# Optimization experiments

Hardware: AMD Instinct MI355X
Metric: run time of the kernel (lower is better)

## Reference

```python
import jax, jax.numpy as jnp
import numpy as np

EPS = 1e-12  # F.normalize eps

def _unfold3(x):
    # x: [B,C,H,W] -> [B, C*9, H*W], matching F.unfold(kernel=3, padding=1)
    B, C, H, W = x.shape
    xp = jnp.pad(x, ((0, 0), (0, 0), (1, 1), (1, 1)))
    pats = jnp.stack([xp[:, :, i:i + H, j:j + W]
                      for i in range(3) for j in range(3)], axis=2)  # [B,C,9,H,W]
    return pats.reshape(B, C * 9, H * W)

def _fold3(t, H, W):
    # inverse of _unfold3 with overlap-add, matching F.fold(kernel=3, padding=1)
    B, CK, L = t.shape
    C = CK // 9
    t = t.reshape(B, C, 3, 3, H, W)
    out = jnp.zeros((B, C, H + 2, W + 2), t.dtype)
    for i in range(3):
        for j in range(3):
            out = out.at[:, :, i:i + H, j:j + W].add(t[:, :, i, j])
    return out[:, :, 1:1 + H, 1:1 + W]

def setup_inputs() -> dict:
    key = jax.random.key(0)
    kV, kK, kQ = jax.random.split(key, 3)
    B, C, H, W = 4, 64, 64, 64
    return {
        'V': jax.random.normal(kV, (B, C, H, W), dtype=jnp.float32),
        'K': jax.random.normal(kK, (B, C, H, W), dtype=jnp.float32),
        'Q': jax.random.normal(kQ, (B, C, H, W), dtype=jnp.float32),
    }

def reference(V, K, Q):
    B, C, H, W = Q.shape
    Qu = _unfold3(Q)  # [B, C9, L]
    Ku = _unfold3(K)  # [B, C9, L]
    # F.normalize along the feature (C*9) axis for both K (after permute dim=2) and Q (dim=1)
    Kn = Ku / jnp.maximum(jnp.linalg.norm(Ku, axis=1, keepdims=True), EPS)
    Qn = Qu / jnp.maximum(jnp.linalg.norm(Qu, axis=1, keepdims=True), EPS)
    # R[b,k,q] = <Kn[b,:,k], Qn[b,:,q]>  -> [B, L, L]
    R = jnp.einsum('bfk,bfq->bkq', Kn, Qn)
    S = jnp.max(R, axis=1)        # [B, L]
    arg = jnp.argmax(R, axis=1)   # [B, L] best key patch per query position
    Vu = _unfold3(V)              # [B, C9, L]
    idx = jnp.broadcast_to(arg[:, None, :], Vu.shape)
    T_unfold = jnp.take_along_axis(Vu, idx, axis=2)  # gather along patch dim
    T = _fold3(T_unfold, H, W) / 9.0                 # [B, C, H, W]
    S = S.reshape(B, 1, H, W)
    return (S, T)
```

## Files before the change

kernel.cpp:

```cpp
#include <hip/hip_runtime.h>
#include <math.h>

#define HW 4096

typedef short bf16x8 __attribute__((ext_vector_type(8)));
typedef float floatx4 __attribute__((ext_vector_type(4)));
typedef unsigned short u16x8 __attribute__((ext_vector_type(8)));

__device__ __forceinline__ unsigned short f2bf_rne(float x) {
    unsigned int u = __float_as_uint(x);
    unsigned int r = (u + 0x7FFFu + ((u >> 16) & 1u)) >> 16;
    return (unsigned short)r;
}
__device__ __forceinline__ float bf2f(unsigned short h) {
    return __uint_as_float(((unsigned int)h) << 16);
}

__device__ __forceinline__ void gload_lds16(const void* gptr, void* lptr) {
    auto g = (const __attribute__((address_space(1))) unsigned int*)(unsigned long long)(gptr);
    auto l = (__attribute__((address_space(3))) unsigned int*)(unsigned int)(unsigned long long)(lptr);
    __builtin_amdgcn_global_load_lds(g, l, 16, 0, 0);
}

__global__ __launch_bounds__(256)
void prep_kernel(const float* __restrict__ Q, const float* __restrict__ K,
                 const float* __restrict__ V,
                 unsigned short* __restrict__ Aq, unsigned short* __restrict__ Bq,
                 float* __restrict__ VT,
                 float* __restrict__ pix2q, float* __restrict__ pix2k) {
    __shared__ float sT[64][65];
    const int tid = threadIdx.x;
    const int p0 = blockIdx.x * 64;
    const int b = blockIdx.y;
    const int which = blockIdx.z;
    const float* __restrict__ src = (which == 0) ? Q : ((which == 1) ? K : V);

#pragma unroll
    for (int it = 0; it < 16; ++it) {
        int idx = it * 256 + tid;
        int c = idx >> 6, x = idx & 63;
        sT[c][x] = src[((size_t)b * 64 + c) * HW + p0 + x];
    }
    __syncthreads();
    const int pp = tid >> 2, qt = tid & 3;

    if (which == 2) {
        float* dst = VT + ((size_t)b * 4096 + p0 + pp) * 64 + qt * 16;
#pragma unroll
        for (int j = 0; j < 4; ++j) {
            float4 v = make_float4(sT[qt * 16 + 4 * j + 0][pp], sT[qt * 16 + 4 * j + 1][pp],
                                   sT[qt * 16 + 4 * j + 2][pp], sT[qt * 16 + 4 * j + 3][pp]);
            *(float4*)(dst + 4 * j) = v;
        }
        return;
    }

    const int isK = which;
    unsigned short* __restrict__ dst = isK ? Bq : Aq;
    float* __restrict__ pix2 = isK ? pix2k : pix2q;
    const size_t base = ((size_t)b * 4096 + p0 + pp) * 192;
    {
        float sq = 0.f;
        u16x8 hv[2], lv[2];
#pragma unroll
        for (int g = 0; g < 2; ++g)
#pragma unroll
            for (int j = 0; j < 8; ++j) {
                int c = qt * 16 + g * 8 + j;
                float x = sT[c][pp];
                sq = fmaf(x, x, sq);
                unsigned short h = f2bf_rne(x);
                hv[g][j] = h;
                lv[g][j] = f2bf_rne(x - bf2f(h));
            }
        sq += __shfl_xor(sq, 1, 64);
        sq += __shfl_xor(sq, 2, 64);
        if (qt == 0) pix2[(b << 12) + p0 + pp] = sq;
#pragma unroll
        for (int g = 0; g < 2; ++g) {
            int co = qt * 16 + g * 8;
            *(u16x8*)(dst + base + co)                     = hv[g];
            *(u16x8*)(dst + base + (isK ? 64 : 128) + co)  = lv[g];
        }
    }
}

__global__ void patchnorm_kernel(const float* __restrict__ pix2q, const float* __restrict__ pix2k,
                                 float* __restrict__ rnq, float* __restrict__ rnk) {
    int idx = blockIdx.x * 256 + threadIdx.x;
    int b = idx >> 12, p = idx & 4095;
    int py = p >> 6, px = p & 63;
    float sq = 0.f, sk = 0.f;
    for (int dy = -1; dy <= 1; ++dy)
        for (int dx = -1; dx <= 1; ++dx) {
            int yy = py + dy, xx = px + dx;
            if ((unsigned)yy < 64u && (unsigned)xx < 64u) {
                int o = (b << 12) + (yy << 6) + xx;
                sq += pix2q[o];
                sk += pix2k[o];
            }
        }
    rnq[idx] = 1.f / fmaxf(sqrtf(sq), 1e-12f);
    rnk[idx] = 1.f / fmaxf(sqrtf(sk), 1e-12f);
}

#define WAITV(n_) asm volatile("s_waitcnt vmcnt(" #n_ ")" ::: "memory")
#define SB do { __builtin_amdgcn_s_barrier(); asm volatile("" ::: "memory"); } while (0)

#define AHB 0
#define ALB 40960
#define BHB 81920
#define BLB 122880
#define SLOT5(u_) ((u_) >= 5 ? (u_) - 5 : (u_))

#define ISS4(c_) do { \
    const size_t ro_ = (size_t)((c_) * 64 + rr) * 384; \
    gload_lds16(agb + ro_ +   0 + G16, smem + AHB + ((c_) % 5) * 8192 + t16); \
    gload_lds16(agb + ro_ + 256 + G16, smem + ALB + ((c_) % 5) * 8192 + t16); \
    gload_lds16(bgb + ro_ +   0 + G16, smem + BHB + ((c_) % 5) * 8192 + t16); \
    gload_lds16(bgb + ro_ + 128 + G16, smem + BLB + ((c_) % 5) * 8192 + t16); \
} while (0)

#define GISS4(c_) do { \
    const size_t ro_ = (size_t)((c_) * 64 + rr) * 384; \
    uint4 va_ = make_uint4(0u,0u,0u,0u), vl_ = va_, wh_ = va_, wl_ = va_; \
    if ((unsigned)(arow + (c_) * 64 + rr) < 4096u) { \
        va_ = *(const uint4*)(agb + ro_ + G16); \
        vl_ = *(const uint4*)(agb + ro_ + 256 + G16); } \
    if ((unsigned)(brow + (c_) * 64 + rr) < 4096u) { \
        wh_ = *(const uint4*)(bgb + ro_ + G16); \
        wl_ = *(const uint4*)(bgb + ro_ + 128 + G16); } \
    *(uint4*)(smem + AHB + ((c_) % 5) * 8192 + t16) = va_; \
    *(uint4*)(smem + ALB + ((c_) % 5) * 8192 + t16) = vl_; \
    *(uint4*)(smem + BHB + ((c_) % 5) * 8192 + t16) = wh_; \
    *(uint4*)(smem + BLB + ((c_) % 5) * 8192 + t16) = wl_; \
} while (0)

#define MM16(af_, bf_, mo_) do { \
    __builtin_amdgcn_s_setprio(1); \
    _Pragma("unroll") \
    for (int mt_ = 0; mt_ < 4; ++mt_) \
        _Pragma("unroll") \
        for (int nt_ = 0; nt_ < 4; ++nt_) \
            acc[(mo_) + mt_][nt_] = __builtin_amdgcn_mfma_f32_16x16x32_bf16( \
                (af_)[mt_], (bf_)[nt_], acc[(mo_) + mt_][nt_], 0, 0, 0); \
    __builtin_amdgcn_s_setprio(0); \
} while (0)

#define LD4(dst_, base_, pk_) do { \
    _Pragma("unroll") \
    for (int q_ = 0; q_ < 4; ++q_) \
        (dst_)[q_] = *(const bf16x8*)((base_) + q_ * 2048 + (pk_)); \
} while (0)

#define DY_STEP(dy_) do { \
    const int sa0_ = SLOT5(wm2 * 2 + (dy_)); \
    const int sa1_ = SLOT5(wm2 * 2 + (dy_) + 1); \
    const int sb_  = SLOT5(wn + (dy_)); \
    const char* Ah0_ = smem + AHB + sa0_ * 8192 + m15 * 128; \
    const char* Ah1_ = smem + AHB + sa1_ * 8192 + m15 * 128; \
    const char* Al0_ = smem + ALB + sa0_ * 8192 + m15 * 128; \
    const char* Al1_ = smem + ALB + sa1_ * 8192 + m15 * 128; \
    const char* Bh_  = smem + BHB + sb_ * 8192 + m15 * 128; \
    const char* Bl_  = smem + BLB + sb_ * 8192 + m15 * 128; \
    _Pragma("unroll") \
    for (int kk = 0; kk < 2; ++kk) { \
        const int pk_ = kk ? posK1 : posK0; \
        bf16x8 bfc[4], bl[4]; \
        LD4(bfc, Bh_, pk_); \
        LD4(bl, Bl_, pk_); \
        { bf16x8 a0[4]; LD4(a0, Ah0_, pk_); MM16(a0, bfc, 0); MM16(a0, bl, 0); } \
        { bf16x8 a1[4]; LD4(a1, Al0_, pk_); MM16(a1, bfc, 0); } \
        { bf16x8 a2[4]; LD4(a2, Ah1_, pk_); MM16(a2, bfc, 4); MM16(a2, bl, 4); } \
        { bf16x8 a3[4]; LD4(a3, Al1_, pk_); MM16(a3, bfc, 4); } \
    } \
} while (0)

__global__ __launch_bounds__(512, 2)
void gemm_fused_kernel(const unsigned short* __restrict__ Aq, const unsigned short* __restrict__ Bq,
                       const float* __restrict__ rnkA,
                       float* __restrict__ part_val, int* __restrict__ part_arg) {
    __shared__ __align__(16) char smem[163840];
    const int tid = threadIdx.x;
    const int lane = tid & 63, wid = tid >> 6;
    const int m15 = lane & 15, quad = lane >> 4;
    const int wn = wid & 3, wm2 = wid >> 2;
    const int f = blockIdx.x;
    const int o = ((f & 7) << 5) + (f >> 3);
    const int kt = o & 15, qt = o >> 4;
    const int k0 = kt << 8, q0 = qt << 8;
    const int b = blockIdx.y;
    const int arow = q0 - 64, brow = k0 - 64;
    const char* agb = (const char*)(Aq + (size_t)b * 4096 * 192) + (ptrdiff_t)arow * 384;
    const char* bgb = (const char*)(Bq + (size_t)b * 4096 * 192) + (ptrdiff_t)brow * 384;
    const bool aInt = (q0 >= 64) && (q0 + 320 <= 4096);
    const bool bInt = (k0 >= 64) && (k0 + 320 <= 4096);

    const int rr = tid >> 3;
    const int G16 = ((tid & 7) ^ (rr & 7)) * 16;
    const int t16 = tid * 16;
    const int posK0 = (quad ^ (m15 & 7)) * 16;
    const int posK1 = ((4 + quad) ^ (m15 & 7)) * 16;

    floatx4 acc[8][4];
#pragma unroll
    for (int i = 0; i < 8; ++i)
#pragma unroll
        for (int j = 0; j < 4; ++j) acc[i][j] = (floatx4)0.f;

    if (aInt && bInt) {
        ISS4(0); ISS4(1); ISS4(2); ISS4(3);
        ISS4(4);
        WAITV(4); SB;
        DY_STEP(0);
        SB;
        ISS4(5);
        WAITV(4); SB;
        DY_STEP(1);
        SB; WAITV(0); SB;
        DY_STEP(2);
        __syncthreads();
    } else {
        GISS4(0); GISS4(1); GISS4(2); GISS4(3);
        __syncthreads();
        DY_STEP(0);
        __syncthreads();
        GISS4(4);
        __syncthreads();
        DY_STEP(1);
        __syncthreads();
        GISS4(5);
        __syncthreads();
        DY_STEP(2);
        __syncthreads();
    }

    float* Csh = (float*)smem;
    float* bvs = (float*)(smem + 66816);
    int*   bas = (int*)(smem + 68864);
    const int q_l = tid & 63;
    const int qr = tid >> 6;
    const int c0 = qr * 32;
    const float4 zero4 = make_float4(0.f, 0.f, 0.f, 0.f);

#pragma unroll
    for (int h = 0; h < 4; ++h) {
        if (h) __syncthreads();
        if (wm2 == (h >> 1)) {
#pragma unroll
            for (int mt2 = 0; mt2 < 4; ++mt2) {
                const int mt = ((h & 1) << 2) + mt2;
#pragma unroll
                for (int nt = 0; nt < 4; ++nt)
#pragma unroll
                    for (int j = 0; j < 4; ++j)
                        Csh[(mt2 * 16 + quad * 4 + j) * 261 + (wn << 6) + nt * 16 + m15] =
                            acc[mt][nt][j];
            }
        }
        __syncthreads();

        const bool qm = q_l > 0;
        const bool qp = q_l < 63;
        const float* rC = Csh + q_l * 261;
        const float* rM = Csh + (q_l - 1) * 261;
        const float* rP = Csh + (q_l + 1) * 261;
        float4 prevm = (qm && c0 > 0) ? *(const float4*)&rM[c0 - 4] : zero4;
        float4 rpj   = qp ? *(const float4*)&rP[c0] : zero4;
        float bv = -INFINITY;
        int ba = 0;
#pragma unroll
        for (int j = 0; j < 8; ++j) {
            int c = c0 + 4 * j;
            float4 cen = *(const float4*)&rC[c];
            float4 rm4 = qm ? *(const float4*)&rM[c] : zero4;
            float4 rp1 = (qp && (c + 4) < 256) ? *(const float4*)&rP[c + 4] : zero4;
            float4 o4;
            o4.x = cen.x + (((c & 63) != 0) ? prevm.w : 0.f) + rpj.y;
            o4.y = cen.y + rm4.x + rpj.z;
            o4.z = cen.z + rm4.y + rpj.w;
            o4.w = cen.w + rm4.z + ((((c + 3) & 63) != 63) ? rp1.x : 0.f);
            float4 rk = *(const float4*)&rnkA[(b << 12) + k0 + c];
            float v0 = o4.x * rk.x; if (v0 > bv) { bv = v0; ba = k0 + c + 0; }
            float v1 = o4.y * rk.y; if (v1 > bv) { bv = v1; ba = k0 + c + 1; }
            float v2 = o4.z * rk.z; if (v2 > bv) { bv = v2; ba = k0 + c + 2; }
            float v3 = o4.w * rk.w; if (v3 > bv) { bv = v3; ba = k0 + c + 3; }
            prevm = rm4;
            rpj = rp1;
        }
        bvs[(qr << 6) + q_l] = bv;
        bas[(qr << 6) + q_l] = ba;
        __syncthreads();
        if (tid < 64) {
            float v = bvs[tid];
            int a = bas[tid];
#pragma unroll
            for (int s = 1; s < 8; ++s) {
                float v2 = bvs[(s << 6) + tid];
                if (v2 > v) { v = v2; a = bas[(s << 6) + tid]; }
            }
            int q = q0 + (h << 6) + tid;
            part_val[(((b << 4) + kt) << 12) + q] = v;
            part_arg[(((b << 4) + kt) << 12) + q] = a;
        }
    }
}

__global__ __launch_bounds__(256)
void argcombine_kernel(const float* __restrict__ part_val, const int* __restrict__ part_arg,
                       const float* __restrict__ rnqA,
                       float* __restrict__ S_out, int* __restrict__ argF) {
    __shared__ float rv[4][64];
    __shared__ int ra[4][64];
    const int tid = threadIdx.x;
    const int qi = tid & 63, sg = tid >> 6;
    const int q = blockIdx.x * 64 + qi;
    const int b = blockIdx.y;
    const int base = (b << 16) + q;
    float bv = -INFINITY; int ba = 0;
#pragma unroll
    for (int i = 0; i < 4; ++i) {
        int s = sg * 4 + i;
        float v = part_val[base + (s << 12)];
        int aa = part_arg[base + (s << 12)];
        if (v > bv) { bv = v; ba = aa; }
    }
    rv[sg][qi] = bv; ra[sg][qi] = ba;
    __syncthreads();
    if (tid < 64) {
        float v = rv[0][tid]; int a = ra[0][tid];
#pragma unroll
        for (int s = 1; s < 4; ++s) {
            float v2 = rv[s][tid];
            if (v2 > v) { v = v2; a = ra[s][tid]; }
        }
        int idx = (b << 12) + blockIdx.x * 64 + tid;
        S_out[idx] = v * rnqA[idx];
        argF[idx] = a;
    }
}

__global__ __launch_bounds__(256)
void gatherT_kernel(const float* __restrict__ VT, const int* __restrict__ argF,
                    float* __restrict__ T_out) {
    __shared__ int sArg[192];
    const int y = blockIdx.x, b = blockIdx.y, cg = blockIdx.z;
    const int tid = threadIdx.x;
    if (tid < 192) {
        int r = tid >> 6, x = tid & 63;
        int yy = y - 1 + r;
        sArg[tid] = ((unsigned)yy < 64u) ? argF[(b << 12) + (yy << 6) + x] : 0;
    }
    __syncthreads();

    const int x = tid >> 2, cq = tid & 3;
    const float* Vb = VT + (size_t)b * 4096 * 64 + cg * 16 + cq * 4;
    float ax = 0.f, ay = 0.f, az = 0.f, aw = 0.f;
#pragma unroll
    for (int t = 0; t < 9; ++t) {
        int dy = t / 3 - 1, dx = t % 3 - 1;
        int qy = y - dy, qx = x - dx;
        if ((unsigned)qy < 64u && (unsigned)qx < 64u) {
            int a = sArg[(1 - dy) * 64 + qx];
            int sy = (a >> 6) + dy, sx = (a & 63) + dx;
            if ((unsigned)sy < 64u && (unsigned)sx < 64u) {
                float4 v = *(const float4*)(Vb + (size_t)((sy << 6) + sx) * 64);
                ax += v.x; ay += v.y; az += v.z; aw += v.w;
            }
        }
    }
    float* Tb = T_out + ((size_t)b * 64 + cg * 16 + cq * 4) * HW + (y << 6) + x;
    Tb[0]          = ax * (1.f / 9.f);
    Tb[HW]         = ay * (1.f / 9.f);
    Tb[2 * HW]     = az * (1.f / 9.f);
    Tb[3 * HW]     = aw * (1.f / 9.f);
}

extern "C" void kernel_launch(void* const* d_in, const int* in_sizes, int n_in,
                              void* d_out, int out_size, void* d_ws, size_t ws_size,
                              hipStream_t stream) {
    const float* V = (const float*)d_in[0];
    const float* K = (const float*)d_in[1];
    const float* Q = (const float*)d_in[2];
    float* S_out = (float*)d_out;
    float* T_out = S_out + 4 * HW;

    char* ws = (char*)d_ws;
    float* pix2q = (float*)(ws + 0);
    float* pix2k = (float*)(ws + 65536);
    float* rnq   = (float*)(ws + 131072);
    float* rnk   = (float*)(ws + 196608);
    float* part_val = (float*)(ws + 262144);
    int*   argF  = (int*)(ws + 4456448);
    int*   part_arg = (int*)(ws + 8650752);
    float* VT    = (float*)(ws + 10747904);
    unsigned short* Aq = (unsigned short*)(ws + 17039360);
    unsigned short* Bq = (unsigned short*)(ws + 23330816);

    prep_kernel<<<dim3(64, 4, 3), 256, 0, stream>>>(Q, K, V, Aq, Bq, VT, pix2q, pix2k);
    patchnorm_kernel<<<64, 256, 0, stream>>>(pix2q, pix2k, rnq, rnk);
    gemm_fused_kernel<<<dim3(256, 4), 512, 0, stream>>>(Aq, Bq, rnk, part_val, part_arg);
    argcombine_kernel<<<dim3(64, 4), 256, 0, stream>>>(part_val, part_arg, rnq, S_out, argF);
    gatherT_kernel<<<dim3(64, 4, 4), 256, 0, stream>>>(VT, argF, T_out);
}
```

Before: 210.6 us.

## Fuse patch norms and argmax combine into GEMM and gather kernels, widen GEMM to 1024 threads

Removes the separate patchnorm and argcombine launches. The key inverse norms are now computed in LDS inside the GEMM epilogue, and the query norm plus the 16-way partial argmax reduction move into the gather kernel's prologue. The GEMM block grows from 8 to 16 waves, each owning a 64x64 tile with half the accumulators, while only the first 512 threads issue loads. This saves launch overhead and global round trips, but it risks register and occupancy pressure: __launch_bounds__(1024,4) with 160KB of LDS is unrealistic. The gather kernel also repeats the partial reduction in every channel-group block.

New measurement: 247.8 us. +17.7%, slower.

```diff
diff --git a/kernel.cpp b/kernel.cpp
--- a/kernel.cpp
+++ b/kernel.cpp
@@ -85,25 +85,6 @@
     }
 }
 
-__global__ void patchnorm_kernel(const float* __restrict__ pix2q, const float* __restrict__ pix2k,
-                                 float* __restrict__ rnq, float* __restrict__ rnk) {
-    int idx = blockIdx.x * 256 + threadIdx.x;
-    int b = idx >> 12, p = idx & 4095;
-    int py = p >> 6, px = p & 63;
-    float sq = 0.f, sk = 0.f;
-    for (int dy = -1; dy <= 1; ++dy)
-        for (int dx = -1; dx <= 1; ++dx) {
-            int yy = py + dy, xx = px + dx;
-            if ((unsigned)yy < 64u && (unsigned)xx < 64u) {
-                int o = (b << 12) + (yy << 6) + xx;
-                sq += pix2q[o];
-                sk += pix2k[o];
-            }
-        }
-    rnq[idx] = 1.f / fmaxf(sqrtf(sq), 1e-12f);
-    rnk[idx] = 1.f / fmaxf(sqrtf(sk), 1e-12f);
-}
-
 #define WAITV(n_) asm volatile("s_waitcnt vmcnt(" #n_ ")" ::: "memory")
 #define SB do { __builtin_amdgcn_s_barrier(); asm volatile("" ::: "memory"); } while (0)
 
@@ -111,39 +92,38 @@
 #define ALB 40960
 #define BHB 81920
 #define BLB 122880
-#define SLOT5(u_) ((u_) >= 5 ? (u_) - 5 : (u_))
-
-#define ISS4(c_) do { \
+
+#define ISSUE4(c_) do { if (issuer) { \
     const size_t ro_ = (size_t)((c_) * 64 + rr) * 384; \
     gload_lds16(agb + ro_ +   0 + G16, smem + AHB + ((c_) % 5) * 8192 + t16); \
     gload_lds16(agb + ro_ + 256 + G16, smem + ALB + ((c_) % 5) * 8192 + t16); \
     gload_lds16(bgb + ro_ +   0 + G16, smem + BHB + ((c_) % 5) * 8192 + t16); \
     gload_lds16(bgb + ro_ + 128 + G16, smem + BLB + ((c_) % 5) * 8192 + t16); \
-} while (0)
-
-#define GISS4(c_) do { \
-    const size_t ro_ = (size_t)((c_) * 64 + rr) * 384; \
-    uint4 va_ = make_uint4(0u,0u,0u,0u), vl_ = va_, wh_ = va_, wl_ = va_; \
+} } while (0)
+
+#define GISS4(c_) do { if (issuer) { \
+    const ptrdiff_t ro_ = (ptrdiff_t)((c_) * 64 + rr) * 384; \
+    uint4 ah_ = make_uint4(0u,0u,0u,0u), al_ = ah_, bh_ = ah_, bl_ = ah_; \
     if ((unsigned)(arow + (c_) * 64 + rr) < 4096u) { \
-        va_ = *(const uint4*)(agb + ro_ + G16); \
-        vl_ = *(const uint4*)(agb + ro_ + 256 + G16); } \
+        ah_ = *(const uint4*)(agb + ro_ + G16); \
+        al_ = *(const uint4*)(agb + ro_ + 256 + G16); } \
     if ((unsigned)(brow + (c_) * 64 + rr) < 4096u) { \
-        wh_ = *(const uint4*)(bgb + ro_ + G16); \
-        wl_ = *(const uint4*)(bgb + ro_ + 128 + G16); } \
-    *(uint4*)(smem + AHB + ((c_) % 5) * 8192 + t16) = va_; \
-    *(uint4*)(smem + ALB + ((c_) % 5) * 8192 + t16) = vl_; \
-    *(uint4*)(smem + BHB + ((c_) % 5) * 8192 + t16) = wh_; \
-    *(uint4*)(smem + BLB + ((c_) % 5) * 8192 + t16) = wl_; \
-} while (0)
-
-#define MM16(af_, bf_, mo_) do { \
+        bh_ = *(const uint4*)(bgb + ro_ + G16); \
+        bl_ = *(const uint4*)(bgb + ro_ + 128 + G16); } \
+    *(uint4*)(smem + AHB + ((c_) % 5) * 8192 + t16) = ah_; \
+    *(uint4*)(smem + ALB + ((c_) % 5) * 8192 + t16) = al_; \
+    *(uint4*)(smem + BHB + ((c_) % 5) * 8192 + t16) = bh_; \
+    *(uint4*)(smem + BLB + ((c_) % 5) * 8192 + t16) = bl_; \
+} } while (0)
+
+#define MM16(af_, bf_) do { \
     __builtin_amdgcn_s_setprio(1); \
     _Pragma("unroll") \
     for (int mt_ = 0; mt_ < 4; ++mt_) \
         _Pragma("unroll") \
         for (int nt_ = 0; nt_ < 4; ++nt_) \
-            acc[(mo_) + mt_][nt_] = __builtin_amdgcn_mfma_f32_16x16x32_bf16( \
-                (af_)[mt_], (bf_)[nt_], acc[(mo_) + mt_][nt_], 0, 0, 0); \
+            acc[mt_][nt_] = __builtin_amdgcn_mfma_f32_16x16x32_bf16( \
+                (af_)[mt_], (bf_)[nt_], acc[mt_][nt_], 0, 0, 0); \
     __builtin_amdgcn_s_setprio(0); \
 } while (0)
 
@@ -154,31 +134,27 @@
 } while (0)
 
 #define DY_STEP(dy_) do { \
-    const int sa0_ = SLOT5(wm2 * 2 + (dy_)); \
-    const int sa1_ = SLOT5(wm2 * 2 + (dy_) + 1); \
-    const int sb_  = SLOT5(wn + (dy_)); \
-    const char* Ah0_ = smem + AHB + sa0_ * 8192 + m15 * 128; \
-    const char* Ah1_ = smem + AHB + sa1_ * 8192 + m15 * 128; \
-    const char* Al0_ = smem + ALB + sa0_ * 8192 + m15 * 128; \
-    const char* Al1_ = smem + ALB + sa1_ * 8192 + m15 * 128; \
-    const char* Bh_  = smem + BHB + sb_ * 8192 + m15 * 128; \
-    const char* Bl_  = smem + BLB + sb_ * 8192 + m15 * 128; \
-    _Pragma("unroll") \
+    const char* Ahs_ = smem + AHB + ((wm2 + (dy_)) % 5) * 8192 + rowB; \
+    const char* Als_ = smem + ALB + ((wm2 + (dy_)) % 5) * 8192 + rowB; \
+    const char* Bhs_ = smem + BHB + ((wn  + (dy_)) % 5) * 8192 + rowB; \
+    const char* Bls_ = smem + BLB + ((wn  + (dy_)) % 5) * 8192 + rowB; \
+    _Pragma("unroll 1") \
     for (int kk = 0; kk < 2; ++kk) { \
         const int pk_ = kk ? posK1 : posK0; \
-        bf16x8 bfc[4], bl[4]; \
-        LD4(bfc, Bh_, pk_); \
-        LD4(bl, Bl_, pk_); \
-        { bf16x8 a0[4]; LD4(a0, Ah0_, pk_); MM16(a0, bfc, 0); MM16(a0, bl, 0); } \
-        { bf16x8 a1[4]; LD4(a1, Al0_, pk_); MM16(a1, bfc, 0); } \
-        { bf16x8 a2[4]; LD4(a2, Ah1_, pk_); MM16(a2, bfc, 4); MM16(a2, bl, 4); } \
-        { bf16x8 a3[4]; LD4(a3, Al1_, pk_); MM16(a3, bfc, 4); } \
+        bf16x8 af[4], bh[4], t4[4]; \
+        LD4(af, Ahs_, pk_); \
+        LD4(bh, Bhs_, pk_); \
+        MM16(af, bh); \
+        LD4(t4, Bls_, pk_); \
+        MM16(af, t4); \
+        LD4(t4, Als_, pk_); \
+        MM16(t4, bh); \
     } \
 } while (0)
 
-__global__ __launch_bounds__(512, 2)
+__global__ __launch_bounds__(1024, 4)
 void gemm_fused_kernel(const unsigned short* __restrict__ Aq, const unsigned short* __restrict__ Bq,
-                       const float* __restrict__ rnkA,
+                       const float* __restrict__ pix2k,
                        float* __restrict__ part_val, int* __restrict__ part_arg) {
     __shared__ __align__(16) char smem[163840];
     const int tid = threadIdx.x;
@@ -196,67 +172,76 @@
     const bool aInt = (q0 >= 64) && (q0 + 320 <= 4096);
     const bool bInt = (k0 >= 64) && (k0 + 320 <= 4096);
 
+    const bool issuer = tid < 512;
     const int rr = tid >> 3;
     const int G16 = ((tid & 7) ^ (rr & 7)) * 16;
     const int t16 = tid * 16;
+    const int rowB = m15 * 128;
     const int posK0 = (quad ^ (m15 & 7)) * 16;
     const int posK1 = ((4 + quad) ^ (m15 & 7)) * 16;
 
-    floatx4 acc[8][4];
-#pragma unroll
-    for (int i = 0; i < 8; ++i)
+    floatx4 acc[4][4];
+#pragma unroll
+    for (int i = 0; i < 4; ++i)
 #pragma unroll
         for (int j = 0; j < 4; ++j) acc[i][j] = (floatx4)0.f;
 
     if (aInt && bInt) {
-        ISS4(0); ISS4(1); ISS4(2); ISS4(3);
-        ISS4(4);
+        ISSUE4(0); ISSUE4(1); ISSUE4(2); ISSUE4(3);
+        ISSUE4(4);
         WAITV(4); SB;
         DY_STEP(0);
         SB;
-        ISS4(5);
+        ISSUE4(5);
         WAITV(4); SB;
         DY_STEP(1);
-        SB; WAITV(0); SB;
+        WAITV(0); SB;
         DY_STEP(2);
-        __syncthreads();
     } else {
-        GISS4(0); GISS4(1); GISS4(2); GISS4(3);
+        GISS4(0); GISS4(1); GISS4(2); GISS4(3); GISS4(4);
         __syncthreads();
         DY_STEP(0);
         __syncthreads();
-        GISS4(4);
+        GISS4(5);
         __syncthreads();
         DY_STEP(1);
-        __syncthreads();
-        GISS4(5);
-        __syncthreads();
         DY_STEP(2);
-        __syncthreads();
-    }
+    }
+    __syncthreads();
 
     float* Csh = (float*)smem;
     float* bvs = (float*)(smem + 66816);
-    int*   bas = (int*)(smem + 68864);
+    int*   bas = (int*)(smem + 70912);
+    float* Lrnk = (float*)(smem + 75008);
+    if (tid < 256) {
+        int k = k0 + tid;
+        int py = k >> 6, px = k & 63;
+        float sk = 0.f;
+        for (int dy = -1; dy <= 1; ++dy)
+            for (int dx = -1; dx <= 1; ++dx) {
+                int yy = py + dy, xx = px + dx;
+                if ((unsigned)yy < 64u && (unsigned)xx < 64u)
+                    sk += pix2k[(b << 12) + (yy << 6) + xx];
+            }
+        Lrnk[tid] = 1.f / fmaxf(sqrtf(sk), 1e-12f);
+    }
     const int q_l = tid & 63;
     const int qr = tid >> 6;
-    const int c0 = qr * 32;
+    const int c0 = qr * 16;
     const float4 zero4 = make_float4(0.f, 0.f, 0.f, 0.f);
 
 #pragma unroll
     for (int h = 0; h < 4; ++h) {
         if (h) __syncthreads();
-        if (wm2 == (h >> 1)) {
-#pragma unroll
-            for (int mt2 = 0; mt2 < 4; ++mt2) {
-                const int mt = ((h & 1) << 2) + mt2;
+        if (wm2 == h) {
+#pragma unroll
+            for (int mt = 0; mt < 4; ++mt)
 #pragma unroll
                 for (int nt = 0; nt < 4; ++nt)
 #pragma unroll
                     for (int j = 0; j < 4; ++j)
-                        Csh[(mt2 * 16 + quad * 4 + j) * 261 + (wn << 6) + nt * 16 + m15] =
+                        Csh[(mt * 16 + quad * 4 + j) * 261 + (wn << 6) + nt * 16 + m15] =
                             acc[mt][nt][j];
-            }
         }
         __syncthreads();
 
@@ -270,7 +255,7 @@
         float bv = -INFINITY;
         int ba = 0;
 #pragma unroll
-        for (int j = 0; j < 8; ++j) {
+        for (int j = 0; j < 4; ++j) {
             int c = c0 + 4 * j;
             float4 cen = *(const float4*)&rC[c];
             float4 rm4 = qm ? *(const float4*)&rM[c] : zero4;
@@ -280,7 +265,7 @@
             o4.y = cen.y + rm4.x + rpj.z;
             o4.z = cen.z + rm4.y + rpj.w;
             o4.w = cen.w + rm4.z + ((((c + 3) & 63) != 63) ? rp1.x : 0.f);
-            float4 rk = *(const float4*)&rnkA[(b << 12) + k0 + c];
+            float4 rk = *(const float4*)&Lrnk[c];
             float v0 = o4.x * rk.x; if (v0 > bv) { bv = v0; ba = k0 + c + 0; }
             float v1 = o4.y * rk.y; if (v1 > bv) { bv = v1; ba = k0 + c + 1; }
             float v2 = o4.z * rk.z; if (v2 > bv) { bv = v2; ba = k0 + c + 2; }
@@ -295,7 +280,7 @@
             float v = bvs[tid];
             int a = bas[tid];
 #pragma unroll
-            for (int s = 1; s < 8; ++s) {
+            for (int s = 1; s < 16; ++s) {
                 float v2 = bvs[(s << 6) + tid];
                 if (v2 > v) { v = v2; a = bas[(s << 6) + tid]; }
             }
@@ -307,49 +292,40 @@
 }
 
 __global__ __launch_bounds__(256)
-void argcombine_kernel(const float* __restrict__ part_val, const int* __restrict__ part_arg,
-                       const float* __restrict__ rnqA,
-                       float* __restrict__ S_out, int* __restrict__ argF) {
-    __shared__ float rv[4][64];
-    __shared__ int ra[4][64];
-    const int tid = threadIdx.x;
-    const int qi = tid & 63, sg = tid >> 6;
-    const int q = blockIdx.x * 64 + qi;
-    const int b = blockIdx.y;
-    const int base = (b << 16) + q;
-    float bv = -INFINITY; int ba = 0;
-#pragma unroll
-    for (int i = 0; i < 4; ++i) {
-        int s = sg * 4 + i;
-        float v = part_val[base + (s << 12)];
-        int aa = part_arg[base + (s << 12)];
-        if (v > bv) { bv = v; ba = aa; }
-    }
-    rv[sg][qi] = bv; ra[sg][qi] = ba;
-    __syncthreads();
-    if (tid < 64) {
-        float v = rv[0][tid]; int a = ra[0][tid];
-#pragma unroll
-        for (int s = 1; s < 4; ++s) {
-            float v2 = rv[s][tid];
-            if (v2 > v) { v = v2; a = ra[s][tid]; }
-        }
-        int idx = (b << 12) + blockIdx.x * 64 + tid;
-        S_out[idx] = v * rnqA[idx];
-        argF[idx] = a;
-    }
-}
-
-__global__ __launch_bounds__(256)
-void gatherT_kernel(const float* __restrict__ VT, const int* __restrict__ argF,
-                    float* __restrict__ T_out) {
+void gatherT_kernel(const float* __restrict__ VT,
+                    const float* __restrict__ part_val, const int* __restrict__ part_arg,
+                    const float* __restrict__ pix2q,
+                    float* __restrict__ S_out, float* __restrict__ T_out) {
     __shared__ int sArg[192];
     const int y = blockIdx.x, b = blockIdx.y, cg = blockIdx.z;
     const int tid = threadIdx.x;
     if (tid < 192) {
         int r = tid >> 6, x = tid & 63;
         int yy = y - 1 + r;
-        sArg[tid] = ((unsigned)yy < 64u) ? argF[(b << 12) + (yy << 6) + x] : 0;
+        int a = 0;
+        if ((unsigned)yy < 64u) {
+            int base = (b << 16) + (yy << 6) + x;
+            float bv = -INFINITY; int ba = 0;
+#pragma unroll
+            for (int s = 0; s < 16; ++s) {
+                float v = part_val[base + (s << 12)];
+                int aa = part_arg[base + (s << 12)];
+                if (v > bv) { bv = v; ba = aa; }
+            }
+            a = ba;
+            if (r == 1 && cg == 0) {
+                float sq = 0.f;
+                for (int dy = -1; dy <= 1; ++dy)
+                    for (int dx = -1; dx <= 1; ++dx) {
+                        int y2 = yy + dy, x2 = x + dx;
+                        if ((unsigned)y2 < 64u && (unsigned)x2 < 64u)
+                            sq += pix2q[(b << 12) + (y2 << 6) + x2];
+                    }
+                S_out[(b << 12) + (yy << 6) + x] =
+                    bv * (1.f / fmaxf(sqrtf(sq), 1e-12f));
+            }
+        }
+        sArg[tid] = a;
     }
     __syncthreads();
 
@@ -388,18 +364,13 @@
     char* ws = (char*)d_ws;
     float* pix2q = (float*)(ws + 0);
     float* pix2k = (float*)(ws + 65536);
-    float* rnq   = (float*)(ws + 131072);
-    float* rnk   = (float*)(ws + 196608);
     float* part_val = (float*)(ws + 262144);
-    int*   argF  = (int*)(ws + 4456448);
     int*   part_arg = (int*)(ws + 8650752);
     float* VT    = (float*)(ws + 10747904);
     unsigned short* Aq = (unsigned short*)(ws + 17039360);
     unsigned short* Bq = (unsigned short*)(ws + 23330816);
 
     prep_kernel<<<dim3(64, 4, 3), 256, 0, stream>>>(Q, K, V, Aq, Bq, VT, pix2q, pix2k);
-    patchnorm_kernel<<<64, 256, 0, stream>>>(pix2q, pix2k, rnq, rnk);
-    gemm_fused_kernel<<<dim3(256, 4), 512, 0, stream>>>(Aq, Bq, rnk, part_val, part_arg);
-    argcombine_kernel<<<dim3(64, 4), 256, 0, stream>>>(part_val, part_arg, rnq, S_out, argF);
-    gatherT_kernel<<<dim3(64, 4, 4), 256, 0, stream>>>(VT, argF, T_out);
-}
+    gemm_fused_kernel<<<dim3(256, 4), 1024, 0, stream>>>(Aq, Bq, pix2k, part_val, part_arg);
+    gatherT_kernel<<<dim3(64, 4, 4), 256, 0, stream>>>(VT, part_val, part_arg, pix2q, S_out, T_out);
+}
```
